# Performance work log

Hardware: AMD Instinct MI355X
Metric: run time of the kernel (lower is better)

Reference implementation:

```python
import jax, jax.numpy as jnp
import numpy as np

N = 50000   # nodes
E = 600000  # edges (before self loops)
D = 128     # in = hidden = out channels
EPS = 1e-5


def setup_inputs() -> dict:
    key = jax.random.key(0)
    ks = jax.random.split(key, 12)
    s = 1.0 / np.sqrt(D)
    inp = {
        "x": jax.random.normal(ks[0], (N, D), jnp.float32),
        "edge_index": jax.random.randint(ks[1], (2, E), 0, N, dtype=jnp.int64),
        "W1": jax.random.normal(ks[2], (D, D), jnp.float32) * s,
        "b1": jnp.zeros((D,), jnp.float32),
        "g1": jnp.ones((D,), jnp.float32),
        "be1": jnp.zeros((D,), jnp.float32),
        "W2": jax.random.normal(ks[3], (D, D), jnp.float32) * s,
        "b2": jnp.zeros((D,), jnp.float32),
        "g2": jnp.ones((D,), jnp.float32),
        "be2": jnp.zeros((D,), jnp.float32),
        "W3": jax.random.normal(ks[4], (D, D), jnp.float32) * s,
        "b3": jnp.zeros((D,), jnp.float32),
    }
    return inp


def _layer_norm(h, g, b):
    mu = jnp.mean(h, axis=-1, keepdims=True)
    var = jnp.mean(jnp.square(h - mu), axis=-1, keepdims=True)
    return (h - mu) * jax.lax.rsqrt(var + EPS) * g + b


def _gcn_layer(h, src, dst, ew, W, b, fill):
    # PyG gcn_norm: append internal self loops with weight `fill`
    loop = jnp.arange(N, dtype=src.dtype)
    s = jnp.concatenate([src, loop])
    d = jnp.concatenate([dst, loop])
    w = jnp.concatenate([ew, jnp.full((N,), fill, h.dtype)])
    deg = jax.ops.segment_sum(w, d, num_segments=N)
    dinv = jnp.where(deg > 0, jax.lax.rsqrt(deg), 0.0)
    norm = dinv[s] * w * dinv[d]  # [E_tot]
    hw = h @ W                    # [N, D]
    out = jax.ops.segment_sum(norm[:, None] * hw[s], d, num_segments=N)
    return out + b


def reference(x, edge_index, W1, b1, g1, be1, W2, b2, g2, be2, W3, b3):
    # outer add_self_loops with edge_weight = 1 (edge_attr is None path)
    loop = jnp.arange(N, dtype=edge_index.dtype)
    src = jnp.concatenate([edge_index[0], loop])
    dst = jnp.concatenate([edge_index[1], loop])
    ew = jnp.ones((E + N,), x.dtype)

    residual = x
    h = _gcn_layer(x, src, dst, ew, W1, b1, 2.0)   # improved=True
    h = jax.nn.relu(_layer_norm(h, g1, be1))
    h = _gcn_layer(h, src, dst, ew, W2, b2, 2.0)   # improved=True
    h = jax.nn.relu(_layer_norm(h, g2, be2))
    h = _gcn_layer(h, src, dst, ew, W3, b3, 1.0)   # improved=False
    return h + residual
```

## Files before the change

kernel.cpp:

```cpp
#include <hip/hip_runtime.h>
#include <hip/hip_bf16.h>
#include <cstdint>

#define N_NODES 50000
#define N_EDGES 600000
#define DCH     128
#define LN_EPS  1e-5f
#define CAP     64
#define CAPSH   6
#define BCAP    16
#define SLICE_N (N_NODES + 1)

typedef __attribute__((ext_vector_type(8))) __bf16 bf16x8;
typedef __attribute__((ext_vector_type(4))) float  f32x4;
typedef __attribute__((ext_vector_type(8))) unsigned short u16x8;
typedef __attribute__((ext_vector_type(2))) unsigned int uint2e;

__device__ inline unsigned short f2bf(float f) {
    unsigned int b; __builtin_memcpy(&b, &f, 4);
    b = b + 0x7fffu + ((b >> 16) & 1u);
    return (unsigned short)(b >> 16);
}
__device__ inline float bf_lo(unsigned int u) {
    unsigned int t = u << 16; float f; __builtin_memcpy(&f, &t, 4); return f;
}
__device__ inline float bf_hi(unsigned int u) {
    unsigned int t = u & 0xffff0000u; float f; __builtin_memcpy(&f, &t, 4); return f;
}

__global__ __launch_bounds__(256) void fill_k(const int* __restrict__ ei,
                                              int* __restrict__ cnt4,
                                              unsigned short* __restrict__ csr) {
    __shared__ int sbad;
    int tid = threadIdx.x;
    if (tid == 0) sbad = 0;
    __syncthreads();
    const long long* e64 = (const long long*)ei;
    long long v = e64[tid];
    long long w = e64[300000 + tid];
    if (v < 0 || v >= N_NODES || w < 0 || w >= N_NODES) sbad = 1;
    __syncthreads();
    int is64 = (sbad == 0);

    int e = blockIdx.x * 256 + tid;
    if (e >= N_EDGES) return;
    long long sv = is64 ? e64[e]           : (long long)ei[e];
    long long dv = is64 ? e64[N_EDGES + e] : (long long)ei[N_EDGES + e];
    int s = (int)(sv < 0 ? 0 : (sv >= N_NODES ? N_NODES - 1 : sv));
    int d = (int)(dv < 0 ? 0 : (dv >= N_NODES ? N_NODES - 1 : dv));
    int b = e & 3;
    int pos = atomicAdd(&cnt4[b * N_NODES + d], 1);
    if (pos < BCAP) csr[(d << CAPSH) + (b << 4) + pos] = (unsigned short)s;
}

#define CVT_T    ((N_NODES + 1) * 32)
#define DINV_OFF CVT_T
#define TRAN_OFF (DINV_OFF + N_NODES)
#define SENT_OFF (TRAN_OFF + 3 * 128 * 128)
#define PREP_T   (SENT_OFF + 128)

__global__ __launch_bounds__(256) void prep_k(
        const float* __restrict__ x, const int* __restrict__ cnt4,
        const float* __restrict__ W1, const float* __restrict__ W2,
        const float* __restrict__ W3,
        unsigned short* __restrict__ xbf, float* __restrict__ dinv2,
        float* __restrict__ dinv1, unsigned short* __restrict__ Wt,
        unsigned short* __restrict__ hbuf) {
    int id = blockIdx.x * 256 + threadIdx.x;
    if (id < CVT_T) {
        int node = id >> 5;
        int co = (id & 31) * 4;
        int slice = co >> 5, off = co & 31;
        uint2 r; r.x = 0u; r.y = 0u;
        if (node < N_NODES) {
            float4 v = *(const float4*)(x + (size_t)node * DCH + co);
            int c = cnt4[node] + cnt4[N_NODES + node]
                  + cnt4[2 * N_NODES + node] + cnt4[3 * N_NODES + node];
            float d = rsqrtf((float)c + 3.0f);
            r.x = ((unsigned int)f2bf(v.y * d) << 16) | (unsigned int)f2bf(v.x * d);
            r.y = ((unsigned int)f2bf(v.w * d) << 16) | (unsigned int)f2bf(v.z * d);
        }
        *(uint2*)(xbf + ((size_t)slice * SLICE_N + node) * 32 + off) = r;
    } else if (id < TRAN_OFF) {
        int i = id - DINV_OFF;
        int c = cnt4[i] + cnt4[N_NODES + i]
              + cnt4[2 * N_NODES + i] + cnt4[3 * N_NODES + i];
        dinv2[i] = rsqrtf((float)c + 3.0f);
        dinv1[i] = rsqrtf((float)c + 2.0f);
    } else if (id < SENT_OFF) {
        int t = id - TRAN_OFF;
        int mat = t >> 14;
        int o = t & 16383;
        int n = o >> 7, k = o & 127;
        const float* W = (mat == 0) ? W1 : ((mat == 1) ? W2 : W3);
        Wt[t] = f2bf(W[k * 128 + n]);
    } else if (id < PREP_T) {
        int i = id - SENT_OFF;
        hbuf[((size_t)(i >> 5) * SLICE_N + N_NODES) * 32 + (i & 31)] = 0;
    }
}

__global__ __launch_bounds__(128) void agg_k(
        const unsigned short* __restrict__ hs, unsigned short* __restrict__ outb,
        const int* __restrict__ cnt4, const unsigned short* __restrict__ csr,
        const float* __restrict__ dinv, float fillp1) {
    int slice = blockIdx.x & 3;
    int grp   = blockIdx.x >> 2;
    int wv    = threadIdx.x >> 6;
    int lane  = threadIdx.x & 63;
    int g     = lane >> 3;
    int l8    = lane & 7;
    int node  = grp * 16 + wv * 8 + g;

    const uint2* hp = (const uint2*)(hs + (size_t)slice * SLICE_N * 32);
    float di = dinv[node];
    int bc0 = min(cnt4[node], BCAP);
    int bc1 = min(cnt4[N_NODES + node], BCAP);
    int bc2 = min(cnt4[2 * N_NODES + node], BCAP);
    int bc3 = min(cnt4[3 * N_NODES + node], BCAP);

    const u16x8* pcsr = (const u16x8*)(csr + ((size_t)node << CAPSH));
    u16x8 c0 = __builtin_nontemporal_load(pcsr + 0);
    u16x8 c1 = __builtin_nontemporal_load(pcsr + 2);
    u16x8 c2 = __builtin_nontemporal_load(pcsr + 4);
    u16x8 c3 = __builtin_nontemporal_load(pcsr + 6);

    float a[4][4];
    #pragma unroll
    for (int k = 0; k < 4; k++)
        #pragma unroll
        for (int ch = 0; ch < 4; ch++) a[k][ch] = 0.f;

    int eidx[32];
    #pragma unroll
    for (int j = 0; j < 8; j++) {
        eidx[j]      = (j < bc0) ? (int)c0[j] : N_NODES;
        eidx[8 + j]  = (j < bc1) ? (int)c1[j] : N_NODES;
        eidx[16 + j] = (j < bc2) ? (int)c2[j] : N_NODES;
        eidx[24 + j] = (j < bc3) ? (int)c3[j] : N_NODES;
    }
    #pragma unroll
    for (int t = 0; t < 32; t++) {
        uint2 u = hp[(size_t)eidx[t] * 8 + l8];
        int k = t & 3;
        a[k][0] += bf_lo(u.x); a[k][1] += bf_hi(u.x);
        a[k][2] += bf_lo(u.y); a[k][3] += bf_hi(u.y);
    }

    int bm = max(max(bc0, bc1), max(bc2, bc3));
    if (__any(bm > 8)) {
        u16x8 d0 = __builtin_nontemporal_load(pcsr + 1);
        u16x8 d1 = __builtin_nontemporal_load(pcsr + 3);
        u16x8 d2 = __builtin_nontemporal_load(pcsr + 5);
        u16x8 d3 = __builtin_nontemporal_load(pcsr + 7);
        int fidx[32];
        #pragma unroll
        for (int j = 0; j < 8; j++) {
            fidx[j]      = (8 + j < bc0) ? (int)d0[j] : N_NODES;
            fidx[8 + j]  = (8 + j < bc1) ? (int)d1[j] : N_NODES;
            fidx[16 + j] = (8 + j < bc2) ? (int)d2[j] : N_NODES;
            fidx[24 + j] = (8 + j < bc3) ? (int)d3[j] : N_NODES;
        }
        #pragma unroll
        for (int t = 0; t < 32; t++) {
            uint2 u = hp[(size_t)fidx[t] * 8 + l8];
            int k = t & 3;
            a[k][0] += bf_lo(u.x); a[k][1] += bf_hi(u.x);
            a[k][2] += bf_lo(u.y); a[k][3] += bf_hi(u.y);
        }
    }

    float s0 = (a[0][0] + a[1][0]) + (a[2][0] + a[3][0]);
    float s1 = (a[0][1] + a[1][1]) + (a[2][1] + a[3][1]);
    float s2 = (a[0][2] + a[1][2]) + (a[2][2] + a[3][2]);
    float s3 = (a[0][3] + a[1][3]) + (a[2][3] + a[3][3]);
    uint2 us = hp[(size_t)node * 8 + l8];
    s0 = di * (s0 + fillp1 * bf_lo(us.x));
    s1 = di * (s1 + fillp1 * bf_hi(us.x));
    s2 = di * (s2 + fillp1 * bf_lo(us.y));
    s3 = di * (s3 + fillp1 * bf_hi(us.y));
    uint2e res;
    res.x = ((unsigned int)f2bf(s1) << 16) | (unsigned int)f2bf(s0);
    res.y = ((unsigned int)f2bf(s3) << 16) | (unsigned int)f2bf(s2);
    __builtin_nontemporal_store(res,
        (uint2e*)(outb + (size_t)slice * SLICE_N * 32) + (size_t)node * 8 + l8);
}


template<int MODE>
__global__ __launch_bounds__(256) void gemm_k(
        const unsigned short* __restrict__ A,
        const unsigned short* __restrict__ Wt,
        const float* __restrict__ bias,
        const float* __restrict__ gamma,
        const float* __restrict__ beta,
        const float* __restrict__ dnext,
        const float* __restrict__ resid,
        unsigned short* __restrict__ out_bf,
        float* __restrict__ out_f) {
    int lane = threadIdx.x & 63;
    int wv   = threadIdx.x >> 6;
    int r0   = (blockIdx.x * 4 + wv) * 16;
    int m = lane & 15, q = lane >> 4;

    bf16x8 afr[4];
    int arow = r0 + m; if (arow >= N_NODES) arow = N_NODES - 1;
    #pragma unroll
    for (int kt = 0; kt < 4; kt++)
        afr[kt] = __builtin_nontemporal_load(
            (const bf16x8*)(A + ((size_t)kt * SLICE_N + arow) * 32 + q * 8));

    f32x4 acc[8];
    #pragma unroll
    for (int nt = 0; nt < 8; nt++) {
        f32x4 c0 = {0.f, 0.f, 0.f, 0.f};
        const unsigned short* bp = Wt + (size_t)(nt * 16 + m) * DCH + q * 8;
        #pragma unroll
        for (int kt = 0; kt < 4; kt++) {
            bf16x8 bfr = *(const bf16x8*)(bp + kt * 32);
            c0 = __builtin_amdgcn_mfma_f32_16x16x32_bf16(afr[kt], bfr, c0, 0, 0, 0);
        }
        acc[nt] = c0;
    }

    float bv[8];
    #pragma unroll
    for (int nt = 0; nt < 8; nt++) bv[nt] = bias[nt * 16 + m];

    if (MODE == 0) {
        float gv[8], bev[8];
        #pragma unroll
        for (int nt = 0; nt < 8; nt++) { gv[nt] = gamma[nt*16+m]; bev[nt] = beta[nt*16+m]; }
        #pragma unroll
        for (int nt = 0; nt < 8; nt++)
            #pragma unroll
            for (int r = 0; r < 4; r++) acc[nt][r] += bv[nt];
        #pragma unroll
        for (int r = 0; r < 4; r++) {
            float s = 0.f, qs = 0.f;
            #pragma unroll
            for (int nt = 0; nt < 8; nt++) { float v = acc[nt][r]; s += v; qs += v*v; }
            #pragma unroll
            for (int msk = 1; msk < 16; msk <<= 1) {
                s  += __shfl_xor(s,  msk, 16);
                qs += __shfl_xor(qs, msk, 16);
            }
            float mean = s * (1.f / 128.f);
            float var  = fmaxf(qs * (1.f / 128.f) - mean * mean, 0.f);
            float rstd = rsqrtf(var + LN_EPS);
            int row = r0 + q * 4 + r;
            if (row < N_NODES) {
                float dscale = dnext[row];
                #pragma unroll
                for (int nt = 0; nt < 8; nt++) {
                    float v = (acc[nt][r] - mean) * rstd * gv[nt] + bev[nt];
                    v = fmaxf(v, 0.f) * dscale;
                    __builtin_nontemporal_store(f2bf(v),
                        out_bf + ((size_t)(nt >> 1) * SLICE_N + row) * 32
                               + (nt & 1) * 16 + m);
                }
            }
        }
    } else {
        #pragma unroll
        for (int r = 0; r < 4; r++) {
            int row = r0 + q * 4 + r;
            if (row < N_NODES) {
                #pragma unroll
                for (int nt = 0; nt < 8; nt++) {
                    float v = acc[nt][r] + bv[nt]
                            + resid[(size_t)row * DCH + nt * 16 + m];
                    out_f[(size_t)row * DCH + nt * 16 + m] = v;
                }
            }
        }
    }
}


extern "C" void kernel_launch(void* const* d_in, const int* in_sizes, int n_in,
                              void* d_out, int out_size, void* d_ws, size_t ws_size,
                              hipStream_t stream) {
    const float* x   = (const float*)d_in[0];
    const int*   ei  = (const int*)d_in[1];
    const float* W1  = (const float*)d_in[2];
    const float* b1  = (const float*)d_in[3];
    const float* g1  = (const float*)d_in[4];
    const float* be1 = (const float*)d_in[5];
    const float* W2  = (const float*)d_in[6];
    const float* b2  = (const float*)d_in[7];
    const float* g2  = (const float*)d_in[8];
    const float* be2 = (const float*)d_in[9];
    const float* W3  = (const float*)d_in[10];
    const float* b3  = (const float*)d_in[11];
    float* out = (float*)d_out;

    char* p = (char*)d_ws;
    auto alloc = [&](size_t bytes) -> void* {
        void* r = (void*)p; p += (bytes + 255) & ~(size_t)255; return r;
    };
    int*   cnt4  = (int*)  alloc((size_t)4 * N_NODES * 4);
    float* dinv2 = (float*)alloc((size_t)N_NODES * 4);
    float* dinv1 = (float*)alloc((size_t)N_NODES * 4);
    unsigned short* csr = (unsigned short*)alloc((size_t)N_NODES * CAP * 2);
    unsigned short* Wt   = (unsigned short*)alloc((size_t)3 * 128 * 128 * 2);
    unsigned short* aggb = (unsigned short*)alloc((size_t)4 * SLICE_N * 32 * 2);
    unsigned short* xbf  = (unsigned short*)alloc((size_t)4 * SLICE_N * 32 * 2);
    unsigned short* hbuf = (unsigned short*)alloc((size_t)4 * SLICE_N * 32 * 2);

    (void)hipMemsetAsync(cnt4, 0, (size_t)4 * N_NODES * 4, stream);
    fill_k<<<(N_EDGES + 255) / 256, 256, 0, stream>>>(ei, cnt4, csr);
    prep_k<<<(PREP_T + 255) / 256, 256, 0, stream>>>(x, cnt4, W1, W2, W3,
                                                     xbf, dinv2, dinv1, Wt, hbuf);

    const int A_BLOCKS = 3125 * 4;
    const int G_BLOCKS = (N_NODES + 63) / 64;

    agg_k<<<A_BLOCKS, 128, 0, stream>>>(xbf, aggb, cnt4, csr, dinv2, 3.0f);
    gemm_k<0><<<G_BLOCKS, 256, 0, stream>>>(aggb, Wt, b1, g1, be1, dinv2, nullptr, hbuf, nullptr);
    agg_k<<<A_BLOCKS, 128, 0, stream>>>(hbuf, aggb, cnt4, csr, dinv2, 3.0f);
    gemm_k<0><<<G_BLOCKS, 256, 0, stream>>>(aggb, Wt + 16384, b2, g2, be2, dinv1, nullptr, hbuf, nullptr);
    agg_k<<<A_BLOCKS, 128, 0, stream>>>(hbuf, aggb, cnt4, csr, dinv1, 2.0f);
    gemm_k<1><<<G_BLOCKS, 256, 0, stream>>>(aggb, Wt + 32768, b3, nullptr, nullptr, nullptr, x, nullptr, out);
}
```

Measured before the change: 325.7 us.

## Cut agg register pressure with staged gathers and 32-row GEMM tiles

The aggregation kernel now gathers neighbours in batches of 16 indices using 32-bit byte offsets instead of 32 size_t indices at once, and adds a min-blocks launch bound. Both aim to lower VGPR use and raise occupancy for the latency-bound gather. The GEMM kernel now has each wave compute two 16-row tiles that share each weight fragment load, halving the block count and weight reloads. In exchange, less gather parallelism is in flight per thread, and the GEMM has fewer blocks, each using more registers.

```diff
diff --git a/kernel.cpp b/kernel.cpp
--- a/kernel.cpp
+++ b/kernel.cpp
@@ -100,7 +100,7 @@
     }
 }
 
-__global__ __launch_bounds__(128) void agg_k(
+__global__ __launch_bounds__(128, 8) void agg_k(
         const unsigned short* __restrict__ hs, unsigned short* __restrict__ outb,
         const int* __restrict__ cnt4, const unsigned short* __restrict__ csr,
         const float* __restrict__ dinv, float fillp1) {
@@ -112,7 +112,8 @@
     int l8    = lane & 7;
     int node  = grp * 16 + wv * 8 + g;
 
-    const uint2* hp = (const uint2*)(hs + (size_t)slice * SLICE_N * 32);
+    const char* hb = (const char*)(hs + (size_t)slice * SLICE_N * 32);
+    unsigned lb = (unsigned)(l8 << 3);
     float di = dinv[node];
     int bc0 = min(cnt4[node], BCAP);
     int bc1 = min(cnt4[N_NODES + node], BCAP);
@@ -120,10 +121,6 @@
     int bc3 = min(cnt4[3 * N_NODES + node], BCAP);
 
     const u16x8* pcsr = (const u16x8*)(csr + ((size_t)node << CAPSH));
-    u16x8 c0 = __builtin_nontemporal_load(pcsr + 0);
-    u16x8 c1 = __builtin_nontemporal_load(pcsr + 2);
-    u16x8 c2 = __builtin_nontemporal_load(pcsr + 4);
-    u16x8 c3 = __builtin_nontemporal_load(pcsr + 6);
 
     float a[4][4];
     #pragma unroll
@@ -131,42 +128,74 @@
         #pragma unroll
         for (int ch = 0; ch < 4; ch++) a[k][ch] = 0.f;
 
-    int eidx[32];
-    #pragma unroll
-    for (int j = 0; j < 8; j++) {
-        eidx[j]      = (j < bc0) ? (int)c0[j] : N_NODES;
-        eidx[8 + j]  = (j < bc1) ? (int)c1[j] : N_NODES;
-        eidx[16 + j] = (j < bc2) ? (int)c2[j] : N_NODES;
-        eidx[24 + j] = (j < bc3) ? (int)c3[j] : N_NODES;
-    }
-    #pragma unroll
-    for (int t = 0; t < 32; t++) {
-        uint2 u = hp[(size_t)eidx[t] * 8 + l8];
-        int k = t & 3;
-        a[k][0] += bf_lo(u.x); a[k][1] += bf_hi(u.x);
-        a[k][2] += bf_lo(u.y); a[k][3] += bf_hi(u.y);
-    }
-
-    int bm = max(max(bc0, bc1), max(bc2, bc3));
-    if (__any(bm > 8)) {
-        u16x8 d0 = __builtin_nontemporal_load(pcsr + 1);
-        u16x8 d1 = __builtin_nontemporal_load(pcsr + 3);
-        u16x8 d2 = __builtin_nontemporal_load(pcsr + 5);
-        u16x8 d3 = __builtin_nontemporal_load(pcsr + 7);
-        int fidx[32];
+    unsigned off[16];
+
+    {
+        u16x8 c0 = __builtin_nontemporal_load(pcsr + 0);
+        u16x8 c1 = __builtin_nontemporal_load(pcsr + 2);
         #pragma unroll
         for (int j = 0; j < 8; j++) {
-            fidx[j]      = (8 + j < bc0) ? (int)d0[j] : N_NODES;
-            fidx[8 + j]  = (8 + j < bc1) ? (int)d1[j] : N_NODES;
-            fidx[16 + j] = (8 + j < bc2) ? (int)d2[j] : N_NODES;
-            fidx[24 + j] = (8 + j < bc3) ? (int)d3[j] : N_NODES;
-        }
-        #pragma unroll
-        for (int t = 0; t < 32; t++) {
-            uint2 u = hp[(size_t)fidx[t] * 8 + l8];
+            off[j]     = ((unsigned)((j < bc0) ? (int)c0[j] : N_NODES) << 6) + lb;
+            off[8 + j] = ((unsigned)((j < bc1) ? (int)c1[j] : N_NODES) << 6) + lb;
+        }
+        #pragma unroll
+        for (int t = 0; t < 16; t++) {
+            uint2 u = *(const uint2*)(hb + off[t]);
             int k = t & 3;
             a[k][0] += bf_lo(u.x); a[k][1] += bf_hi(u.x);
             a[k][2] += bf_lo(u.y); a[k][3] += bf_hi(u.y);
+        }
+    }
+    {
+        u16x8 c2 = __builtin_nontemporal_load(pcsr + 4);
+        u16x8 c3 = __builtin_nontemporal_load(pcsr + 6);
+        #pragma unroll
+        for (int j = 0; j < 8; j++) {
+            off[j]     = ((unsigned)((j < bc2) ? (int)c2[j] : N_NODES) << 6) + lb;
+            off[8 + j] = ((unsigned)((j < bc3) ? (int)c3[j] : N_NODES) << 6) + lb;
+        }
+        #pragma unroll
+        for (int t = 0; t < 16; t++) {
+            uint2 u = *(const uint2*)(hb + off[t]);
+            int k = t & 3;
+            a[k][0] += bf_lo(u.x); a[k][1] += bf_hi(u.x);
+            a[k][2] += bf_lo(u.y); a[k][3] += bf_hi(u.y);
+        }
+    }
+
+    int bm = max(max(bc0, bc1), max(bc2, bc3));
+    if (__any(bm > 8)) {
+        {
+            u16x8 d0 = __builtin_nontemporal_load(pcsr + 1);
+            u16x8 d1 = __builtin_nontemporal_load(pcsr + 3);
+            #pragma unroll
+            for (int j = 0; j < 8; j++) {
+                off[j]     = ((unsigned)((8 + j < bc0) ? (int)d0[j] : N_NODES) << 6) + lb;
+                off[8 + j] = ((unsigned)((8 + j < bc1) ? (int)d1[j] : N_NODES) << 6) + lb;
+            }
+            #pragma unroll
+            for (int t = 0; t < 16; t++) {
+                uint2 u = *(const uint2*)(hb + off[t]);
+                int k = t & 3;
+                a[k][0] += bf_lo(u.x); a[k][1] += bf_hi(u.x);
+                a[k][2] += bf_lo(u.y); a[k][3] += bf_hi(u.y);
+            }
+        }
+        {
+            u16x8 d2 = __builtin_nontemporal_load(pcsr + 5);
+            u16x8 d3 = __builtin_nontemporal_load(pcsr + 7);
+            #pragma unroll
+            for (int j = 0; j < 8; j++) {
+                off[j]     = ((unsigned)((8 + j < bc2) ? (int)d2[j] : N_NODES) << 6) + lb;
+                off[8 + j] = ((unsigned)((8 + j < bc3) ? (int)d3[j] : N_NODES) << 6) + lb;
+            }
+            #pragma unroll
+            for (int t = 0; t < 16; t++) {
+                uint2 u = *(const uint2*)(hb + off[t]);
+                int k = t & 3;
+                a[k][0] += bf_lo(u.x); a[k][1] += bf_hi(u.x);
+                a[k][2] += bf_lo(u.y); a[k][3] += bf_hi(u.y);
+            }
         }
     }
 
@@ -174,7 +203,7 @@
     float s1 = (a[0][1] + a[1][1]) + (a[2][1] + a[3][1]);
     float s2 = (a[0][2] + a[1][2]) + (a[2][2] + a[3][2]);
     float s3 = (a[0][3] + a[1][3]) + (a[2][3] + a[3][3]);
-    uint2 us = hp[(size_t)node * 8 + l8];
+    uint2 us = *(const uint2*)(hb + ((unsigned)node << 6) + lb);
     s0 = di * (s0 + fillp1 * bf_lo(us.x));
     s1 = di * (s1 + fillp1 * bf_hi(us.x));
     s2 = di * (s2 + fillp1 * bf_lo(us.y));
@@ -200,27 +229,31 @@
         float* __restrict__ out_f) {
     int lane = threadIdx.x & 63;
     int wv   = threadIdx.x >> 6;
-    int r0   = (blockIdx.x * 4 + wv) * 16;
+    int r0   = (blockIdx.x * 4 + wv) * 32;
     int m = lane & 15, q = lane >> 4;
 
-    bf16x8 afr[4];
-    int arow = r0 + m; if (arow >= N_NODES) arow = N_NODES - 1;
+    bf16x8 afr[2][4];
     #pragma unroll
-    for (int kt = 0; kt < 4; kt++)
-        afr[kt] = __builtin_nontemporal_load(
-            (const bf16x8*)(A + ((size_t)kt * SLICE_N + arow) * 32 + q * 8));
-
-    f32x4 acc[8];
+    for (int mt = 0; mt < 2; mt++) {
+        int arow = r0 + mt * 16 + m; if (arow >= N_NODES) arow = N_NODES - 1;
+        #pragma unroll
+        for (int kt = 0; kt < 4; kt++)
+            afr[mt][kt] = __builtin_nontemporal_load(
+                (const bf16x8*)(A + ((size_t)kt * SLICE_N + arow) * 32 + q * 8));
+    }
+
+    f32x4 acc[2][8];
     #pragma unroll
     for (int nt = 0; nt < 8; nt++) {
-        f32x4 c0 = {0.f, 0.f, 0.f, 0.f};
+        f32x4 c0 = {0.f,0.f,0.f,0.f}, c1 = {0.f,0.f,0.f,0.f};
         const unsigned short* bp = Wt + (size_t)(nt * 16 + m) * DCH + q * 8;
         #pragma unroll
         for (int kt = 0; kt < 4; kt++) {
             bf16x8 bfr = *(const bf16x8*)(bp + kt * 32);
-            c0 = __builtin_amdgcn_mfma_f32_16x16x32_bf16(afr[kt], bfr, c0, 0, 0, 0);
-        }
-        acc[nt] = c0;
+            c0 = __builtin_amdgcn_mfma_f32_16x16x32_bf16(afr[0][kt], bfr, c0, 0, 0, 0);
+            c1 = __builtin_amdgcn_mfma_f32_16x16x32_bf16(afr[1][kt], bfr, c1, 0, 0, 0);
+        }
+        acc[0][nt] = c0; acc[1][nt] = c1;
     }
 
     float bv[8];
@@ -232,48 +265,53 @@
         #pragma unroll
         for (int nt = 0; nt < 8; nt++) { gv[nt] = gamma[nt*16+m]; bev[nt] = beta[nt*16+m]; }
         #pragma unroll
-        for (int nt = 0; nt < 8; nt++)
-            #pragma unroll
-            for (int r = 0; r < 4; r++) acc[nt][r] += bv[nt];
-        #pragma unroll
-        for (int r = 0; r < 4; r++) {
-            float s = 0.f, qs = 0.f;
-            #pragma unroll
-            for (int nt = 0; nt < 8; nt++) { float v = acc[nt][r]; s += v; qs += v*v; }
-            #pragma unroll
-            for (int msk = 1; msk < 16; msk <<= 1) {
-                s  += __shfl_xor(s,  msk, 16);
-                qs += __shfl_xor(qs, msk, 16);
-            }
-            float mean = s * (1.f / 128.f);
-            float var  = fmaxf(qs * (1.f / 128.f) - mean * mean, 0.f);
-            float rstd = rsqrtf(var + LN_EPS);
-            int row = r0 + q * 4 + r;
-            if (row < N_NODES) {
-                float dscale = dnext[row];
+        for (int mt = 0; mt < 2; mt++) {
+            #pragma unroll
+            for (int nt = 0; nt < 8; nt++)
                 #pragma unroll
-                for (int nt = 0; nt < 8; nt++) {
-                    float v = (acc[nt][r] - mean) * rstd * gv[nt] + bev[nt];
-                    v = fmaxf(v, 0.f) * dscale;
-                    __builtin_nontemporal_store(f2bf(v),
-                        out_bf + ((size_t)(nt >> 1) * SLICE_N + row) * 32
-                               + (nt & 1) * 16 + m);
+                for (int r = 0; r < 4; r++) acc[mt][nt][r] += bv[nt];
+            #pragma unroll
+            for (int r = 0; r < 4; r++) {
+                float s = 0.f, qs = 0.f;
+                #pragma unroll
+                for (int nt = 0; nt < 8; nt++) { float v = acc[mt][nt][r]; s += v; qs += v*v; }
+                #pragma unroll
+                for (int msk = 1; msk < 16; msk <<= 1) {
+                    s  += __shfl_xor(s,  msk, 16);
+                    qs += __shfl_xor(qs, msk, 16);
                 }
+                float mean = s * (1.f / 128.f);
+                float var  = fmaxf(qs * (1.f / 128.f) - mean * mean, 0.f);
+                float rstd = rsqrtf(var + LN_EPS);
+                int row = r0 + mt * 16 + q * 4 + r;
+                if (row < N_NODES) {
+                    float dscale = dnext[row];
+                    #pragma unroll
+                    for (int nt = 0; nt < 8; nt++) {
+                        float v = (acc[mt][nt][r] - mean) * rstd * gv[nt] + bev[nt];
+                        v = fmaxf(v, 0.f) * dscale;
+                        __builtin_nontemporal_store(f2bf(v),
+                            out_bf + ((size_t)(nt >> 1) * SLICE_N + row) * 32
+                                   + (nt & 1) * 16 + m);
+                    }
+                }
             }
         }
     } else {
         #pragma unroll
-        for (int r = 0; r < 4; r++) {
-            int row = r0 + q * 4 + r;
-            if (row < N_NODES) {
-                #pragma unroll
-                for (int nt = 0; nt < 8; nt++) {
-                    float v = acc[nt][r] + bv[nt]
-                            + resid[(size_t)row * DCH + nt * 16 + m];
-                    out_f[(size_t)row * DCH + nt * 16 + m] = v;
+        for (int mt = 0; mt < 2; mt++)
+            #pragma unroll
+            for (int r = 0; r < 4; r++) {
+                int row = r0 + mt * 16 + q * 4 + r;
+                if (row < N_NODES) {
+                    #pragma unroll
+                    for (int nt = 0; nt < 8; nt++) {
+                        float v = acc[mt][nt][r] + bv[nt]
+                                + resid[(size_t)row * DCH + nt * 16 + m];
+                        out_f[(size_t)row * DCH + nt * 16 + m] = v;
+                    }
                 }
             }
-        }
     }
 }
 
@@ -314,7 +352,7 @@
                                                      xbf, dinv2, dinv1, Wt, hbuf);
 
     const int A_BLOCKS = 3125 * 4;
-    const int G_BLOCKS = (N_NODES + 63) / 64;
+    const int G_BLOCKS = (N_NODES + 127) / 128;
 
     agg_k<<<A_BLOCKS, 128, 0, stream>>>(xbf, aggb, cnt4, csr, dinv2, 3.0f);
     gemm_k<0><<<G_BLOCKS, 256, 0, stream>>>(aggb, Wt, b1, g1, be1, dinv2, nullptr, hbuf, nullptr);
```

After: 882.9 us. +171.1%, slower.
